# Performance work log

Measured on AMD Instinct MI355X. Metric: run time of the kernel, lower is better.

## Reference

```python
import jax, jax.numpy as jnp
import numpy as np

NUM_TABLES = 26
VOCAB = 100000
D = 128          # sparse_feature_size == mlp_bot[-1]
B = 8192
P = 10           # fixed pooling factor per bag
DENSE = 13
BOT = [512, 256, 128]
TOP = [1024, 1024, 512, 256, 1]
NF = NUM_TABLES + 1  # features entering dot interaction


def setup_inputs() -> dict:
    key = jax.random.key(0)
    ks = iter(jax.random.split(key, 32))
    inp = {}
    inp["dense_x"] = jax.random.normal(next(ks), (B, DENSE), dtype=jnp.float32)
    inp["sparse_indices"] = jax.random.randint(next(ks), (NUM_TABLES, B * P), 0, VOCAB, dtype=jnp.int32)
    # EmbeddingBag weights init: uniform(-0.01, 0.01)
    inp["emb_tables"] = jax.random.uniform(next(ks), (NUM_TABLES, VOCAB, D), jnp.float32, -0.01, 0.01)
    def xavier(k, shape):
        fan_out, fan_in = shape
        lim = np.sqrt(6.0 / (fan_in + fan_out)).astype(np.float32)
        return jax.random.uniform(k, shape, jnp.float32, -lim, lim)
    dims_bot = [DENSE] + BOT
    for i in range(len(BOT)):
        inp[f"bot_w{i}"] = xavier(next(ks), (dims_bot[i + 1], dims_bot[i]))
        inp[f"bot_b{i}"] = jnp.zeros((dims_bot[i + 1],), jnp.float32)
    interact_dim = NF * (NF - 1) // 2 + BOT[-1]  # 351 + 128 = 479
    dims_top = [interact_dim] + TOP
    for i in range(len(TOP)):
        inp[f"top_w{i}"] = xavier(next(ks), (dims_top[i + 1], dims_top[i]))
        inp[f"top_b{i}"] = jnp.zeros((dims_top[i + 1],), jnp.float32)
    return inp


def reference(dense_x, sparse_indices, emb_tables,
              bot_w0, bot_b0, bot_w1, bot_b1, bot_w2, bot_b2,
              top_w0, top_b0, top_w1, top_b1, top_w2, top_b2,
              top_w3, top_b3, top_w4, top_b4):
    # bottom MLP (Linear + ReLU on every layer)
    x = dense_x
    for w, b in ((bot_w0, bot_b0), (bot_w1, bot_b1), (bot_w2, bot_b2)):
        x = jax.nn.relu(x @ w.T + b)  # [B, 128]

    # multi-table EmbeddingBag sum pooling (fixed pooling factor P)
    idx = sparse_indices.reshape(NUM_TABLES, B, P)
    ly = jax.vmap(lambda tab, i: tab[i].sum(axis=1))(emb_tables, idx)  # [T, B, D]

    # dot interaction: bmm + upper-triangular gather
    T_feat = jnp.concatenate([x[None], ly], axis=0).transpose(1, 0, 2)  # [B, NF, D]
    Z = jnp.einsum('bnd,bmd->bnm', T_feat, T_feat)                       # [B, NF, NF]
    li, lj = np.triu_indices(NF, k=1)
    Zflat = Z[:, li, lj]                                                 # [B, NF*(NF-1)/2]
    z = jnp.concatenate([x, Zflat], axis=1)                              # [B, 479]

    # top MLP: ReLU on all but last layer
    h = z
    tops = ((top_w0, top_b0), (top_w1, top_b1), (top_w2, top_b2), (top_w3, top_b3))
    for w, b in tops:
        h = jax.nn.relu(h @ w.T + b)
    p = h @ top_w4.T + top_b4  # [B, 1]
    return jax.nn.sigmoid(p.squeeze(1))
```

## Files before the change

kernel.cpp:

```cpp
#include <hip/hip_runtime.h>
#include <hip/hip_bf16.h>
#include <cstdint>

typedef __attribute__((ext_vector_type(8))) short bf16x8;
typedef __attribute__((ext_vector_type(4))) short bf16x4;
typedef __attribute__((ext_vector_type(4))) float f32x4;

#define B_SZ 8192
#define TROW 3456

__device__ __forceinline__ void gld_lds16(const void* g, void* l) {
    __builtin_amdgcn_global_load_lds(
        (const __attribute__((address_space(1))) unsigned int*)g,
        (__attribute__((address_space(3))) unsigned int*)l, 16, 0, 0);
}

__device__ __forceinline__ short f2bf_bits(float v) {
    return __builtin_bit_cast(short, __float2bfloat16(v));
}

struct CvtJob { const float* in; __hip_bfloat16* out; int N, K, Kp; };
struct CvtJobs { CvtJob j[6]; int start[7]; };

__device__ __forceinline__ void cvt_dev8(int lb, int tid, const CvtJobs& J) {
    int chunk = lb * 256 + tid;
    int e = chunk * 8;
    if (e >= J.start[6]) return;
    int k = 0;
    #pragma unroll
    for (int i = 1; i < 6; i++) if (e >= J.start[i]) k = i;
    const CvtJob& job = J.j[k];
    int local = e - J.start[k];
    float v[8];
    if (job.K == job.Kp) {
        const float4* p = (const float4*)(job.in + local);
        float4 a = p[0], b = p[1];
        v[0]=a.x; v[1]=a.y; v[2]=a.z; v[3]=a.w; v[4]=b.x; v[5]=b.y; v[6]=b.z; v[7]=b.w;
    } else {
        int n = local / job.Kp, kk = local - n * job.Kp;
        #pragma unroll
        for (int i = 0; i < 8; i++)
            v[i] = (kk + i < job.K) ? job.in[(size_t)n * job.K + kk + i] : 0.f;
    }
    bf16x8 o;
    #pragma unroll
    for (int i = 0; i < 8; i++)
        o[i] = f2bf_bits(v[i]);
    *(bf16x8*)(job.out + local) = o;
}

__device__ __forceinline__ void bot0_dev(int lb, int tid, const float* __restrict__ x,
    const float* __restrict__ w, const float* __restrict__ bias,
    __hip_bfloat16* __restrict__ o, float* xs) {
    int m0 = lb * 4;
    if (tid < 52) xs[tid] = x[(size_t)m0 * 13 + tid];
    __syncthreads();
    for (int c = tid; c < 512; c += 256) {
        const float* wr = w + (size_t)c * 13;
        float bv = bias[c];
        #pragma unroll
        for (int r = 0; r < 4; r++) {
            float s = bv;
            #pragma unroll
            for (int k = 0; k < 13; k++) s += xs[r * 13 + k] * wr[k];
            o[(size_t)(m0 + r) * 512 + c] = __float2bfloat16(fmaxf(s, 0.f));
        }
    }
}

__device__ __forceinline__ void emb_dev(int lb, int tid, int t0,
    const int* __restrict__ idx, const float* __restrict__ tab,
    __hip_bfloat16* __restrict__ T) {
    int lane = tid & 63, wv = tid >> 6;
    int p = lb * 4 + wv;
    int t = t0 + (p >> 13);
    int b = p & 8191;
    const int* ip = idx + (size_t)t * 81920 + b * 10;
    const float* tb = tab + (size_t)t * 100000 * 128;
    int half = lane >> 5, l32 = lane & 31;
    float4 s = {0.f, 0.f, 0.f, 0.f};
    #pragma unroll
    for (int j = 0; j < 10; j += 2) {
        int r = ip[j + half];
        float4 v = ((const float4*)(tb + (size_t)r * 128))[l32];
        s.x += v.x; s.y += v.y; s.z += v.z; s.w += v.w;
    }
    s.x += __shfl_xor(s.x, 32, 64);
    s.y += __shfl_xor(s.y, 32, 64);
    s.z += __shfl_xor(s.z, 32, 64);
    s.w += __shfl_xor(s.w, 32, 64);
    if (half == 0) {
        bf16x4 o;
        o[0] = f2bf_bits(s.x); o[1] = f2bf_bits(s.y);
        o[2] = f2bf_bits(s.z); o[3] = f2bf_bits(s.w);
        ((bf16x4*)(T + (size_t)b * TROW + (1 + t) * 128))[l32] = o;
    }
}

template<int TM, int TN, int WM, int WN>
__device__ __forceinline__ void gemm_dev(int tileId, int nTiles, int nbx, int tid,
    const __hip_bfloat16* __restrict__ A, const __hip_bfloat16* __restrict__ W,
    const float* __restrict__ bias, __hip_bfloat16* __restrict__ C,
    int K, int ldc, __hip_bfloat16* ABs) {
    constexpr int BK = 64;
    constexpr int ROWS = TM + TN;
    constexpr int CH = ROWS * BK / 2048;
    constexpr int MI = TM / WM / 16;
    constexpr int NI = TN / WN / 16;

    int swz = tileId;
    if ((nTiles & 7) == 0) {
        int q = nTiles >> 3;
        swz = (tileId & 7) * q + (tileId >> 3);
    }
    const int by = swz / nbx, bx = swz - by * nbx;
    const int m0 = by * TM, n0 = bx * TN;

    const int lane = tid & 63, wave = tid >> 6;
    const int wmI = wave / WN, wnI = wave % WN;

    const __hip_bfloat16* gp[CH];
    #pragma unroll
    for (int c = 0; c < CH; c++) {
        int gid = c * 256 + tid;
        int row = gid >> 3;
        int cs = ((gid & 7) ^ (row & 7)) * 8;
        gp[c] = (row < TM ? A + (size_t)(m0 + row) * K
                          : W + (size_t)(n0 + row - TM) * K) + cs;
    }

    f32x4 acc[MI][NI] = {};
    const int fr = lane & 15, hi = lane >> 4;

    for (int k0 = 0; k0 < K; k0 += BK) {
        __syncthreads();
        #pragma unroll
        for (int c = 0; c < CH; c++)
            gld_lds16(gp[c] + k0, &ABs[(c * 256 + wave * 64) * 8]);
        asm volatile("s_waitcnt vmcnt(0)" ::: "memory");
        __syncthreads();
        #pragma unroll
        for (int ks = 0; ks < 2; ks++) {
            bf16x8 a[MI], b[NI];
            #pragma unroll
            for (int i = 0; i < MI; i++) {
                int row = wmI * (TM / WM) + i * 16 + fr;
                a[i] = *(const bf16x8*)&ABs[row * BK + (((ks * 4 + hi) ^ (row & 7)) * 8)];
            }
            #pragma unroll
            for (int j = 0; j < NI; j++) {
                int row = TM + wnI * (TN / WN) + j * 16 + fr;
                b[j] = *(const bf16x8*)&ABs[row * BK + (((ks * 4 + hi) ^ (row & 7)) * 8)];
            }
            #pragma unroll
            for (int i = 0; i < MI; i++)
                #pragma unroll
                for (int j = 0; j < NI; j++)
                    acc[i][j] = __builtin_amdgcn_mfma_f32_16x16x32_bf16(a[i], b[j], acc[i][j], 0, 0, 0);
        }
    }

    const int fq = hi;
    #pragma unroll
    for (int i = 0; i < MI; i++) {
        #pragma unroll
        for (int j = 0; j < NI; j++) {
            int n = n0 + wnI * (TN / WN) + j * 16 + fr;
            float bv = bias[n];
            #pragma unroll
            for (int r = 0; r < 4; r++) {
                int m = m0 + wmI * (TM / WM) + i * 16 + fq * 4 + r;
                C[(size_t)m * ldc + n] = __float2bfloat16(fmaxf(acc[i][j][r] + bv, 0.f));
            }
        }
    }
}

template<int TM, int TN, int WM, int WN>
__global__ __launch_bounds__(256) void gemm_k(const __hip_bfloat16* A, const __hip_bfloat16* W,
                                              const float* bias, __hip_bfloat16* C,
                                              int nbx, int K, int ldc) {
    __shared__ __align__(16) __hip_bfloat16 ABs[(TM + TN) * 64];
    gemm_dev<TM, TN, WM, WN>(blockIdx.x, gridDim.x, nbx, threadIdx.x, A, W, bias, C, K, ldc, ABs);
}

__global__ __launch_bounds__(256) void k_pre_emb(CvtJobs J, int cvtB,
    const float* dx, const float* w0, const float* b0, __hip_bfloat16* bufA,
    int t0, const int* sidx, const float* tab, __hip_bfloat16* T) {
    __shared__ float xs[64];
    int blk = blockIdx.x, tid = threadIdx.x;
    if (blk < cvtB) { cvt_dev8(blk, tid, J); return; }
    blk -= cvtB;
    if (blk < B_SZ / 4) { bot0_dev(blk, tid, dx, w0, b0, bufA, xs); return; }
    emb_dev(blk - B_SZ / 4, tid, t0, sidx, tab, T);
}

template<int TM, int TN>
__global__ __launch_bounds__(256) void k_gemm_emb(const __hip_bfloat16* A, const __hip_bfloat16* W,
    const float* bias, __hip_bfloat16* C, int nbx, int K, int ldc, int gB,
    int t0, const int* sidx, const float* tab, __hip_bfloat16* T) {
    __shared__ __align__(16) __hip_bfloat16 ABs[(TM + TN) * 64];
    if (blockIdx.x < gB)
        gemm_dev<TM, TN, 2, 2>(blockIdx.x, gB, nbx, threadIdx.x, A, W, bias, C, K, ldc, ABs);
    else
        emb_dev(blockIdx.x - gB, threadIdx.x, t0, sidx, tab, T);
}

__global__ __launch_bounds__(256) void k_int(const __hip_bfloat16* __restrict__ T,
                                             __hip_bfloat16* __restrict__ z) {
    int lane = threadIdx.x & 63, wave = threadIdx.x >> 6;
    int b = blockIdx.x * 4 + wave;
    const __hip_bfloat16* Tb = T + (size_t)b * TROW;

    const int fr = lane & 15, fkb = (lane >> 4) * 8;
    bf16x8 fr2[2][4];
    #pragma unroll
    for (int mi = 0; mi < 2; mi++)
        #pragma unroll
        for (int kt = 0; kt < 4; kt++)
            fr2[mi][kt] = *(const bf16x8*)&Tb[(mi * 16 + fr) * 128 + kt * 32 + fkb];

    f32x4 acc[2][2] = {};
    #pragma unroll
    for (int kt = 0; kt < 4; kt++)
        #pragma unroll
        for (int mi = 0; mi < 2; mi++)
            #pragma unroll
            for (int ni = 0; ni < 2; ni++)
                acc[mi][ni] = __builtin_amdgcn_mfma_f32_16x16x32_bf16(fr2[mi][kt], fr2[ni][kt], acc[mi][ni], 0, 0, 0);

    __hip_bfloat16* zb = z + (size_t)b * 512;
    ((unsigned*)zb)[lane] = ((const unsigned*)Tb)[lane];
    if (lane < 33) zb[479 + lane] = __float2bfloat16(0.f);
    const int fq = lane >> 4;
    #pragma unroll
    for (int mi = 0; mi < 2; mi++)
        #pragma unroll
        for (int ni = 0; ni < 2; ni++)
            #pragma unroll
            for (int r = 0; r < 4; r++) {
                int m = mi * 16 + fq * 4 + r;
                int n = ni * 16 + fr;
                if (m < 27 && n < 27 && m < n) {
                    int p = m * 26 - (m * (m - 1)) / 2 + (n - m - 1);
                    zb[128 + p] = __float2bfloat16(acc[mi][ni][r]);
                }
            }
}

__global__ __launch_bounds__(256) void k_top3_fin(const __hip_bfloat16* __restrict__ A,
                                                  const __hip_bfloat16* __restrict__ W,
                                                  const float* __restrict__ b3,
                                                  const float* __restrict__ w4,
                                                  const float* __restrict__ b4,
                                                  float* __restrict__ out) {
    constexpr int TM = 64, TN = 256, K = 512;
    constexpr int ROWS = TM + TN;
    constexpr int CH = ROWS * 4 / 256;
    __shared__ __align__(16) __hip_bfloat16 ABs[ROWS * 32];
    __shared__ float red[4 * 64];

    const int tid = threadIdx.x;
    const int lane = tid & 63, wave = tid >> 6;
    const int m0 = blockIdx.x * TM;

    const __hip_bfloat16* gp[CH];
    #pragma unroll
    for (int c = 0; c < CH; c++) {
        int gid = c * 256 + tid;
        int row = gid >> 2, col = (gid & 3) * 8;
        gp[c] = (row < TM ? A + (size_t)(m0 + row) * K
                          : W + (size_t)(row - TM) * K) + col;
    }

    f32x4 acc[4][4] = {};
    const int fr = lane & 15, fkb = (lane >> 4) * 8;

    for (int k0 = 0; k0 < K; k0 += 32) {
        __syncthreads();
        #pragma unroll
        for (int c = 0; c < CH; c++)
            gld_lds16(gp[c] + k0, &ABs[(c * 256 + wave * 64) * 8]);
        asm volatile("s_waitcnt vmcnt(0)" ::: "memory");
        __syncthreads();
        bf16x8 a[4], b[4];
        #pragma unroll
        for (int i = 0; i < 4; i++)
            a[i] = *(const bf16x8*)&ABs[(i * 16 + fr) * 32 + fkb];
        #pragma unroll
        for (int j = 0; j < 4; j++)
            b[j] = *(const bf16x8*)&ABs[(TM + wave * 64 + j * 16 + fr) * 32 + fkb];
        #pragma unroll
        for (int i = 0; i < 4; i++)
            #pragma unroll
            for (int j = 0; j < 4; j++)
                acc[i][j] = __builtin_amdgcn_mfma_f32_16x16x32_bf16(a[i], b[j], acc[i][j], 0, 0, 0);
    }

    float p[4][4] = {};
    #pragma unroll
    for (int j = 0; j < 4; j++) {
        int n = wave * 64 + j * 16 + fr;
        float bv = b3[n], wv = w4[n];
        #pragma unroll
        for (int i = 0; i < 4; i++)
            #pragma unroll
            for (int r = 0; r < 4; r++)
                p[i][r] += fmaxf(acc[i][j][r] + bv, 0.f) * wv;
    }
    #pragma unroll
    for (int mask = 1; mask < 16; mask <<= 1)
        #pragma unroll
        for (int i = 0; i < 4; i++)
            #pragma unroll
            for (int r = 0; r < 4; r++)
                p[i][r] += __shfl_xor(p[i][r], mask, 64);
    const int fq = lane >> 4;
    if (fr == 0) {
        #pragma unroll
        for (int i = 0; i < 4; i++)
            #pragma unroll
            for (int r = 0; r < 4; r++)
                red[wave * 64 + i * 16 + fq * 4 + r] = p[i][r];
    }
    __syncthreads();
    if (tid < 64) {
        float s = red[tid] + red[64 + tid] + red[128 + tid] + red[192 + tid];
        out[m0 + tid] = 1.f / (1.f + expf(-(s + b4[0])));
    }
}

extern "C" void kernel_launch(void* const* d_in, const int* in_sizes, int n_in,
                              void* d_out, int out_size, void* d_ws, size_t ws_size,
                              hipStream_t stream) {
    const float* dense_x = (const float*)d_in[0];
    const int* sidx      = (const int*)d_in[1];
    const float* emb     = (const float*)d_in[2];
    const float* bw0 = (const float*)d_in[3];  const float* bb0 = (const float*)d_in[4];
    const float* bw1 = (const float*)d_in[5];  const float* bb1 = (const float*)d_in[6];
    const float* bw2 = (const float*)d_in[7];  const float* bb2 = (const float*)d_in[8];
    const float* tw0 = (const float*)d_in[9];  const float* tb0 = (const float*)d_in[10];
    const float* tw1 = (const float*)d_in[11]; const float* tb1 = (const float*)d_in[12];
    const float* tw2 = (const float*)d_in[13]; const float* tb2 = (const float*)d_in[14];
    const float* tw3 = (const float*)d_in[15]; const float* tb3 = (const float*)d_in[16];
    const float* tw4 = (const float*)d_in[17]; const float* tb4 = (const float*)d_in[18];
    float* out = (float*)d_out;

    char* ws = (char*)d_ws;
    size_t off = 0;
    auto alloc = [&](size_t bytes) {
        off = (off + 255) & ~(size_t)255;
        void* p = ws + off;
        off += bytes;
        return p;
    };
    __hip_bfloat16* Wb1 = (__hip_bfloat16*)alloc((size_t)256 * 512 * 2);
    __hip_bfloat16* Wb2 = (__hip_bfloat16*)alloc((size_t)128 * 256 * 2);
    __hip_bfloat16* Wt0 = (__hip_bfloat16*)alloc((size_t)1024 * 512 * 2);
    __hip_bfloat16* Wt1 = (__hip_bfloat16*)alloc((size_t)1024 * 1024 * 2);
    __hip_bfloat16* Wt2 = (__hip_bfloat16*)alloc((size_t)512 * 1024 * 2);
    __hip_bfloat16* Wt3 = (__hip_bfloat16*)alloc((size_t)256 * 512 * 2);
    __hip_bfloat16* bufA = (__hip_bfloat16*)alloc((size_t)B_SZ * 512 * 2);
    __hip_bfloat16* bufB = (__hip_bfloat16*)alloc((size_t)B_SZ * 256 * 2);
    __hip_bfloat16* Tbuf = (__hip_bfloat16*)alloc((size_t)B_SZ * TROW * 2);
    __hip_bfloat16* zbuf = (__hip_bfloat16*)alloc((size_t)B_SZ * 512 * 2);
    __hip_bfloat16* h0   = (__hip_bfloat16*)alloc((size_t)B_SZ * 1024 * 2);
    __hip_bfloat16* h1   = (__hip_bfloat16*)alloc((size_t)B_SZ * 1024 * 2);
    __hip_bfloat16* h2   = (__hip_bfloat16*)alloc((size_t)B_SZ * 512 * 2);

    CvtJobs J;
    auto setJob = [&](int i, const float* in, __hip_bfloat16* o, int N, int K, int Kp) {
        J.j[i] = {in, o, N, K, Kp};
    };
    setJob(0, bw1, Wb1, 256, 512, 512);
    setJob(1, bw2, Wb2, 128, 256, 256);
    setJob(2, tw0, Wt0, 1024, 479, 512);
    setJob(3, tw1, Wt1, 1024, 1024, 1024);
    setJob(4, tw2, Wt2, 512, 1024, 1024);
    setJob(5, tw3, Wt3, 256, 512, 512);
    J.start[0] = 0;
    for (int i = 0; i < 6; i++) J.start[i + 1] = J.start[i] + J.j[i].N * J.j[i].Kp;
    const int cvtB = (J.start[6] / 8 + 255) / 256;
    const int EMB_T = B_SZ / 4;

    k_pre_emb<<<cvtB + B_SZ / 4 + 9 * EMB_T, 256, 0, stream>>>(
        J, cvtB, dense_x, bw0, bb0, bufA, 0, sidx, emb, Tbuf);

    k_gemm_emb<128, 64><<<256 + 8 * EMB_T, 256, 0, stream>>>(
        bufA, Wb1, bb1, bufB, 256 / 64, 512, 256, 256, 9, sidx, emb, Tbuf);

    k_gemm_emb<64, 64><<<256 + 9 * EMB_T, 256, 0, stream>>>(
        bufB, Wb2, bb2, Tbuf, 128 / 64, 256, TROW, 256, 17, sidx, emb, Tbuf);

    k_int<<<B_SZ / 4, 256, 0, stream>>>(Tbuf, zbuf);

    gemm_k<128,128, 2, 2><<<(B_SZ / 128) * (1024 / 128), 256, 0, stream>>>(zbuf, Wt0, tb0, h0, 1024 / 128, 512, 1024);
    gemm_k<128,128, 2, 2><<<(B_SZ / 128) * (1024 / 128), 256, 0, stream>>>(h0, Wt1, tb1, h1, 1024 / 128, 1024, 1024);
    gemm_k<128,128, 2, 2><<<(B_SZ / 128) * ( 512 / 128), 256, 0, stream>>>(h1, Wt2, tb2, h2, 512 / 128, 1024, 512);

    k_top3_fin<<<B_SZ / 64, 256, 0, stream>>>(h2, Wt3, tb3, tw4, tb4, out);
}
```

Baseline: 297.8 us.

## Add triple-buffered 256x128 pipelined GEMM for first two top-MLP layers

Introduces a 512-thread GEMM kernel with 256x128 tiles, a three-stage LDS ring filled by direct global-to-LDS loads with prefetch two tiles ahead, XOR-swizzled LDS layout, MFMA priority raising and an XCD-aware block swizzle. It replaces the 128x128 gemm_k for the top MLP layers 0 and 1 to hide global load latency and increase per-block reuse. The larger tile halves the block count (256 blocks) and uses about 144KB of LDS, which limits occupancy to one block per CU.

```diff
diff --git a/kernel.cpp b/kernel.cpp
--- a/kernel.cpp
+++ b/kernel.cpp
@@ -182,6 +182,116 @@
                                               int nbx, int K, int ldc) {
     __shared__ __align__(16) __hip_bfloat16 ABs[(TM + TN) * 64];
     gemm_dev<TM, TN, WM, WN>(blockIdx.x, gridDim.x, nbx, threadIdx.x, A, W, bias, C, K, ldc, ABs);
+}
+
+template<int KTILES>
+__global__ __launch_bounds__(512) void gemm_pipe(const __hip_bfloat16* __restrict__ A,
+                                                 const __hip_bfloat16* __restrict__ W,
+                                                 const float* __restrict__ bias,
+                                                 __hip_bfloat16* __restrict__ C,
+                                                 int nbx, int ldc) {
+    constexpr int K = KTILES * 64;
+    __shared__ __align__(16) __hip_bfloat16 ABs[3 * 384 * 64];
+    const int tid = threadIdx.x;
+    const int lane = tid & 63, wave = tid >> 6;
+    const int wm = wave >> 2, wn = wave & 3;
+
+    int swz = blockIdx.x;
+    { int q = (int)gridDim.x >> 3; swz = (swz & 7) * q + (swz >> 3); }
+    const int by = swz / nbx, bx = swz - by * nbx;
+    const int m0 = by * 256, n0 = bx * 128;
+
+    const __hip_bfloat16* gp[6];
+    #pragma unroll
+    for (int r = 0; r < 6; r++) {
+        int gid = r * 512 + tid;
+        int row = gid >> 3;
+        int cs = ((gid & 7) ^ (row & 7)) * 8;
+        gp[r] = (row < 256 ? A + (size_t)(m0 + row) * K
+                           : W + (size_t)(n0 + row - 256) * K) + cs;
+    }
+    auto stage3 = [&](int s, int t, int r0) {
+        __hip_bfloat16* dst = &ABs[s * 384 * 64];
+        #pragma unroll
+        for (int r = 0; r < 3; r++)
+            gld_lds16(gp[r0 + r] + t * 64, &dst[((r0 + r) * 512 + wave * 64) * 8]);
+    };
+
+    f32x4 acc[8][2] = {};
+    const int fr = lane & 15, hi = lane >> 4;
+
+    stage3(0, 0, 0); stage3(0, 0, 3);
+    stage3(1, 1, 0); stage3(1, 1, 3);
+    asm volatile("s_waitcnt vmcnt(6)" ::: "memory");
+    __builtin_amdgcn_s_barrier();
+
+    for (int t = 0; t < KTILES; ++t) {
+        const __hip_bfloat16* buf = &ABs[(t % 3) * 384 * 64];
+        const bool pf = (t + 2) < KTILES;
+        const int s2 = (t + 2) % 3;
+
+        if (pf) stage3(s2, t + 2, 0);
+        {
+            bf16x8 a[8], b[2];
+            #pragma unroll
+            for (int i = 0; i < 8; i++) {
+                int row = wm * 128 + i * 16 + fr;
+                a[i] = *(const bf16x8*)&buf[row * 64 + ((hi ^ (row & 7)) * 8)];
+            }
+            #pragma unroll
+            for (int j = 0; j < 2; j++) {
+                int row = 256 + wn * 32 + j * 16 + fr;
+                b[j] = *(const bf16x8*)&buf[row * 64 + ((hi ^ (row & 7)) * 8)];
+            }
+            __builtin_amdgcn_s_setprio(1);
+            #pragma unroll
+            for (int i = 0; i < 8; i++)
+                #pragma unroll
+                for (int j = 0; j < 2; j++)
+                    acc[i][j] = __builtin_amdgcn_mfma_f32_16x16x32_bf16(a[i], b[j], acc[i][j], 0, 0, 0);
+            __builtin_amdgcn_s_setprio(0);
+        }
+        __builtin_amdgcn_s_barrier();
+
+        if (pf) stage3(s2, t + 2, 3);
+        {
+            bf16x8 a[8], b[2];
+            #pragma unroll
+            for (int i = 0; i < 8; i++) {
+                int row = wm * 128 + i * 16 + fr;
+                a[i] = *(const bf16x8*)&buf[row * 64 + (((4 + hi) ^ (row & 7)) * 8)];
+            }
+            #pragma unroll
+            for (int j = 0; j < 2; j++) {
+                int row = 256 + wn * 32 + j * 16 + fr;
+                b[j] = *(const bf16x8*)&buf[row * 64 + (((4 + hi) ^ (row & 7)) * 8)];
+            }
+            __builtin_amdgcn_s_setprio(1);
+            #pragma unroll
+            for (int i = 0; i < 8; i++)
+                #pragma unroll
+                for (int j = 0; j < 2; j++)
+                    acc[i][j] = __builtin_amdgcn_mfma_f32_16x16x32_bf16(a[i], b[j], acc[i][j], 0, 0, 0);
+            __builtin_amdgcn_s_setprio(0);
+        }
+        if (pf) asm volatile("s_waitcnt vmcnt(6)" ::: "memory");
+        else    asm volatile("s_waitcnt vmcnt(0)" ::: "memory");
+        __builtin_amdgcn_s_barrier();
+    }
+
+    #pragma unroll
+    for (int i = 0; i < 8; i++) {
+        #pragma unroll
+        for (int j = 0; j < 2; j++) {
+            int n = n0 + wn * 32 + j * 16 + fr;
+            float bv = bias[n];
+            #pragma unroll
+            for (int r = 0; r < 4; r++) {
+                int m = m0 + wm * 128 + i * 16 + hi * 4 + r;
+                C[(size_t)m * ldc + n] = __float2bfloat16(fmaxf(acc[i][j][r] + bv, 0.f));
+            }
+        }
+    }
 }
 
 __global__ __launch_bounds__(256) void k_pre_emb(CvtJobs J, int cvtB,
@@ -394,8 +504,9 @@
 
     k_int<<<B_SZ / 4, 256, 0, stream>>>(Tbuf, zbuf);
 
-    gemm_k<128,128, 2, 2><<<(B_SZ / 128) * (1024 / 128), 256, 0, stream>>>(zbuf, Wt0, tb0, h0, 1024 / 128, 512, 1024);
-    gemm_k<128,128, 2, 2><<<(B_SZ / 128) * (1024 / 128), 256, 0, stream>>>(h0, Wt1, tb1, h1, 1024 / 128, 1024, 1024);
+    gemm_pipe< 8><<<(B_SZ / 256) * (1024 / 128), 512, 0, stream>>>(zbuf, Wt0, tb0, h0, 1024 / 128, 1024);
+    gemm_pipe<16><<<(B_SZ / 256) * (1024 / 128), 512, 0, stream>>>(h0, Wt1, tb1, h1, 1024 / 128, 1024);
+
     gemm_k<128,128, 2, 2><<<(B_SZ / 128) * ( 512 / 128), 256, 0, stream>>>(h1, Wt2, tb2, h2, 512 / 128, 1024, 512);
 
     k_top3_fin<<<B_SZ / 64, 256, 0, stream>>>(h2, Wt3, tb3, tw4, tb4, out);
```

Measured after the change: 287.3 us. 3.5% less time.
